# Kernel tuning notes

Measured on AMD Instinct MI355X. Metric: run time of the kernel, lower is better.

Reference implementation:

```python
import jax, jax.numpy as jnp
import numpy as np

N_NODES = 100000
D_IN = 128
D_OUT = 128
N_REL = 4
N_EDGES = 500000


def setup_inputs() -> dict:
    key = jax.random.key(0)
    k_x, k_e, k_w, k_b, k_ws, k_bs = jax.random.split(key, 6)
    x = jax.random.normal(k_x, (N_NODES, D_IN), dtype=jnp.float32)
    # edge_indices[r] = [2, E]: row 0 = source node ids, row 1 = target node ids
    edge_indices = jax.random.randint(k_e, (N_REL, 2, N_EDGES), 0, N_NODES, dtype=jnp.int32)
    scale = 1.0 / np.sqrt(D_IN)
    # per-relation Linear weights (out, in) and biases, like nn.Linear
    W = jax.random.uniform(k_w, (N_REL, D_OUT, D_IN), dtype=jnp.float32, minval=-scale, maxval=scale)
    b = jax.random.uniform(k_b, (N_REL, D_OUT), dtype=jnp.float32, minval=-scale, maxval=scale)
    W_sl = jax.random.uniform(k_ws, (D_OUT, D_IN), dtype=jnp.float32, minval=-scale, maxval=scale)
    b_sl = jax.random.uniform(k_bs, (D_OUT,), dtype=jnp.float32, minval=-scale, maxval=scale)
    return {"x": x, "edge_indices": edge_indices, "W": W, "b": b, "W_sl": W_sl, "b_sl": b_sl}


def reference(x, edge_indices, W, b, W_sl, b_sl):
    # gather source features per relation: [R, E, D_IN]
    src = edge_indices[:, 0]  # [R, E]
    tgt = edge_indices[:, 1]  # [R, E]
    xs = x[src]  # [R, E, D_IN]
    # per-relation linear (nn.Linear: x @ W.T + b): [R, E, D_OUT]
    msgs = jnp.einsum('red,rfd->ref', xs, W) + b[:, None, :]
    # scatter-add into per-relation node accumulators, then sum over relations
    agg = jax.vmap(lambda m, t: jax.ops.segment_sum(m, t, num_segments=N_NODES))(msgs, tgt)
    agg = agg.sum(axis=0)  # [N, D_OUT]
    # self loop
    agg = agg + x @ W_sl.T + b_sl
    return agg
```

## Files before the change

kernel.cpp:

```cpp
#include <hip/hip_runtime.h>
#include <hip/hip_bf16.h>

#define N_NODES 100000
#define D 128
#define N_REL 4
#define N_EDGES 500000
#define N_CNT (N_REL * N_NODES)
#define SCAN_CHUNK 1024
#define N_SCAN_BLK ((N_CNT + SCAN_CHUNK - 1) / SCAN_CHUNK)
#define SORT_MAX (N_REL * N_EDGES + 3 * N_CNT)
#define NXCD 8
#define NODES_PER_XCD (N_NODES / NXCD)

typedef __attribute__((ext_vector_type(8))) short bf16x8;
typedef __attribute__((ext_vector_type(4))) float f32x4;

__device__ __forceinline__ unsigned short f2bf(float f) {
    unsigned int u = __float_as_uint(f);
    u += 0x7fffu + ((u >> 16) & 1u);
    return (unsigned short)(u >> 16);
}

#define CVT_BLOCKS 6250
#define WB_BLOCKS 320
#define ZR_BLOCKS 1
#define HIST_BLOCKS (7813 * NXCD)
__global__ __launch_bounds__(256) void prep_kernel(const float* __restrict__ x,
                                                   const int* __restrict__ ei,
                                                   const float* __restrict__ W,
                                                   const float* __restrict__ W_sl,
                                                   ushort* __restrict__ xbf,
                                                   ushort* __restrict__ WbT,
                                                   int* __restrict__ cnt) {
    const int b = blockIdx.x, tid = threadIdx.x;
    if (b < CVT_BLOCKS) {
        size_t t = (size_t)b * 256 + tid;
        float4 v0 = ((const float4*)x)[t * 2];
        float4 v1 = ((const float4*)x)[t * 2 + 1];
        int4 o;
        o.x = ((int)f2bf(v0.y) << 16) | f2bf(v0.x);
        o.y = ((int)f2bf(v0.w) << 16) | f2bf(v0.z);
        o.z = ((int)f2bf(v1.y) << 16) | f2bf(v1.x);
        o.w = ((int)f2bf(v1.w) << 16) | f2bf(v1.z);
        ((int4*)xbf)[t] = o;
    } else if (b < CVT_BLOCKS + WB_BLOCKS) {
        int t = (b - CVT_BLOCKS) * 256 + tid;
        int f = t / 640;
        int k = t - f * 640;
        float v;
        if (k < 512) {
            int r = k >> 7, d = k & 127;
            v = W[((size_t)r * 128 + f) * 128 + d];
        } else {
            v = W_sl[(size_t)f * 128 + (k - 512)];
        }
        WbT[t] = f2bf(v);
    } else if (b < CVT_BLOCKS + WB_BLOCKS + ZR_BLOCKS) {
        if (tid < 16) ((uint4*)(xbf + (size_t)N_NODES * D))[tid] = make_uint4(0, 0, 0, 0);
    } else {
        int hb = b - CVT_BLOCKS - WB_BLOCKS - ZR_BLOCKS;
        int xcd = hb & 7;
        int t = (hb >> 3) * 256 + tid;
        if (t >= N_REL * N_EDGES) return;
        int r = t / N_EDGES;
        int e = t - r * N_EDGES;
        int tgt = ei[(size_t)r * 2 * N_EDGES + N_EDGES + e];
        if ((unsigned)(tgt - xcd * NODES_PER_XCD) < (unsigned)NODES_PER_XCD)
            atomicAdd(&cnt[r * N_NODES + tgt], 1);
    }
}

__global__ __launch_bounds__(256) void scanA(const int* __restrict__ cnt,
                                             int* __restrict__ foff,
                                             int* __restrict__ partials) {
    __shared__ int ps[256];
    int b = blockIdx.x, t = threadIdx.x;
    int i0 = b * SCAN_CHUNK + t * 4;
    int v[4];
#pragma unroll
    for (int q = 0; q < 4; ++q) v[q] = (i0 + q < N_CNT) ? ((cnt[i0 + q] + 3) & ~3) : 0;
    int s = v[0] + v[1] + v[2] + v[3];
    ps[t] = s;
    __syncthreads();
    for (int d = 1; d < 256; d <<= 1) {
        int u = (t >= d) ? ps[t - d] : 0;
        __syncthreads();
        ps[t] += u;
        __syncthreads();
    }
    if (t == 255) partials[b] = ps[255];
    int run = (t == 0) ? 0 : ps[t - 1];
#pragma unroll
    for (int q = 0; q < 4; ++q) {
        if (i0 + q < N_CNT) foff[i0 + q] = run;
        run += v[q];
    }
}

__global__ __launch_bounds__(256) void scanC(int* __restrict__ foff,
                                             const int* __restrict__ partials,
                                             const int* __restrict__ cnt,
                                             int* __restrict__ cur0,
                                             int* __restrict__ sorted) {
    __shared__ int red[256];
    const int b = blockIdx.x, t = threadIdx.x;
    const int pb = b >> 2;
    int s = 0;
    for (int j = t; j < pb; j += 256) s += partials[j];
    red[t] = s;
    __syncthreads();
    for (int d = 128; d > 0; d >>= 1) {
        if (t < d) red[t] += red[t + d];
        __syncthreads();
    }
    const int P = red[0];
    int i = b * 256 + t;
    if (i >= N_CNT) return;
    int base = foff[i] + P;
    foff[i] = base;
    cur0[i] = 0;
    int c = cnt[i];
    int cp = (c + 3) & ~3;
    for (int j = c; j < cp; ++j) sorted[base + j] = N_NODES;
    if (i == N_CNT - 1) foff[N_CNT] = base + cp;
}

__global__ __launch_bounds__(256) void bucket_kernel(const int* __restrict__ ei,
                                                     const int* __restrict__ foff,
                                                     int* __restrict__ cur0,
                                                     int* __restrict__ sorted) {
    const int xcd = blockIdx.x & 7;
    int t = (blockIdx.x >> 3) * 256 + threadIdx.x;
    if (t >= N_REL * N_EDGES) return;
    int r = t / N_EDGES;
    int e = t - r * N_EDGES;
    int tgt = ei[(size_t)r * 2 * N_EDGES + N_EDGES + e];
    if ((unsigned)(tgt - xcd * NODES_PER_XCD) >= (unsigned)NODES_PER_XCD) return;
    int src = ei[(size_t)r * 2 * N_EDGES + e];
    int i = r * N_NODES + tgt;
    int pos = foff[i] + atomicAdd(&cur0[i], 1);
    sorted[pos] = src;
}

__global__ __launch_bounds__(256) void gather_kernel(const ushort* __restrict__ xbf,
                                                     const int* __restrict__ sorted,
                                                     const int* __restrict__ foff,
                                                     unsigned int* __restrict__ buf) {
    int wid = (blockIdx.x * 256 + threadIdx.x) >> 6;
    wid = __builtin_amdgcn_readfirstlane(wid);
    const int lane = threadIdx.x & 63;
    const int p0 = wid * 4;
    int f0 = foff[p0], f1 = foff[p0 + 1], f2 = foff[p0 + 2], f3 = foff[p0 + 3], f4 = foff[p0 + 4];
#pragma unroll
    for (int pi = 0; pi < 4; ++pi) {
        int gb = (pi == 0) ? f0 : (pi == 1) ? f1 : (pi == 2) ? f2 : f3;
        int ge = (pi == 0) ? f1 : (pi == 1) ? f2 : (pi == 2) ? f3 : f4;
        float ax = 0.f, ay = 0.f;
        for (int g = gb; g < ge; g += 4) {
            int4 s = *(const int4*)(sorted + g);
            unsigned int u0 = ((const unsigned int*)(xbf + ((size_t)s.x << 7)))[lane];
            unsigned int u1 = ((const unsigned int*)(xbf + ((size_t)s.y << 7)))[lane];
            unsigned int u2 = ((const unsigned int*)(xbf + ((size_t)s.z << 7)))[lane];
            unsigned int u3 = ((const unsigned int*)(xbf + ((size_t)s.w << 7)))[lane];
            ax += __uint_as_float(u0 << 16) + __uint_as_float(u1 << 16)
                + __uint_as_float(u2 << 16) + __uint_as_float(u3 << 16);
            ay += __uint_as_float(u0 & 0xffff0000u) + __uint_as_float(u1 & 0xffff0000u)
                + __uint_as_float(u2 & 0xffff0000u) + __uint_as_float(u3 & 0xffff0000u);
        }
        buf[(size_t)(p0 + pi) * 64 + lane] = ((unsigned int)f2bf(ay) << 16) | f2bf(ax);
    }
}

__global__ __launch_bounds__(256) void gemm_kernel(const ushort* __restrict__ buf,
                                                   const ushort* __restrict__ xbf,
                                                   const ushort* __restrict__ WbT,
                                                   const int* __restrict__ cnt,
                                                   const float* __restrict__ bias,
                                                   const float* __restrict__ b_sl,
                                                   float* __restrict__ out) {
    __shared__ __align__(16) float SH[64 * 132];
    __shared__ float degS[4 * 128];
    __shared__ float biasS[4 * 128];
    __shared__ float bslS[128];
    ushort* As = (ushort*)SH;
    ushort* Bs = As + 128 * 64;

    const int tid = threadIdx.x;
    const int l = tid & 63, w = tid >> 6;
    const int wr = w >> 1, wc = w & 1;
    const int lr = l & 15, lq = l >> 4;
    const int n0 = blockIdx.x * 128;

#pragma unroll
    for (int it = 0; it < 2; ++it) {
        int idx = it * 256 + tid;
        int r = idx >> 7, row = idx & 127;
        int n = n0 + row;
        degS[idx] = (n < N_NODES) ? (float)cnt[r * N_NODES + n] : 0.f;
        biasS[idx] = bias[idx];
    }
    if (tid < 128) bslS[tid] = b_sl[tid];

    f32x4 acc[4][4];
#pragma unroll
    for (int mi = 0; mi < 4; ++mi)
#pragma unroll
        for (int ni = 0; ni < 4; ++ni) acc[mi][ni] = (f32x4){0.f, 0.f, 0.f, 0.f};

    for (int kt = 0; kt < 10; ++kt) {
        __syncthreads();
        const int region = kt >> 1;
        const int d0 = (kt & 1) * 64;
#pragma unroll
        for (int it = 0; it < 4; ++it) {
            int id = it * 256 + tid;
            int r_ = id >> 3, c16 = id & 7;
            int n = n0 + r_;
            if (n > N_NODES - 1) n = N_NODES - 1;
            const ushort* sp = (region < 4)
                ? (buf + (((size_t)region * N_NODES + n) << 7) + d0)
                : (xbf + ((size_t)n << 7) + d0);
            int4 va = *(const int4*)(sp + c16 * 8);
            *(int4*)(As + r_ * 64 + ((c16 ^ (r_ & 7)) << 3)) = va;
            int4 vb = *(const int4*)(WbT + (size_t)r_ * 640 + kt * 64 + c16 * 8);
            *(int4*)(Bs + r_ * 64 + ((c16 ^ (r_ & 7)) << 3)) = vb;
        }
        __syncthreads();
#pragma unroll
        for (int ks = 0; ks < 2; ++ks) {
            const int ch = ks * 4 + lq;
            const int chs = (ch ^ (lr & 7)) << 3;
            bf16x8 a[4], bb[4];
#pragma unroll
            for (int mi = 0; mi < 4; ++mi)
                a[mi] = *(const bf16x8*)(As + (wr * 64 + mi * 16 + lr) * 64 + chs);
#pragma unroll
            for (int ni = 0; ni < 4; ++ni)
                bb[ni] = *(const bf16x8*)(Bs + (wc * 64 + ni * 16 + lr) * 64 + chs);
#pragma unroll
            for (int mi = 0; mi < 4; ++mi)
#pragma unroll
                for (int ni = 0; ni < 4; ++ni)
                    acc[mi][ni] = __builtin_amdgcn_mfma_f32_16x16x32_bf16(a[mi], bb[ni], acc[mi][ni], 0, 0, 0);
        }
    }

    float bw[4][4], bsl_[4];
#pragma unroll
    for (int ni = 0; ni < 4; ++ni) {
        int f = wc * 64 + ni * 16 + lr;
        bsl_[ni] = bslS[f];
#pragma unroll
        for (int r = 0; r < 4; ++r) bw[ni][r] = biasS[r * 128 + f];
    }
    float* Cs = SH;
#pragma unroll
    for (int h = 0; h < 2; ++h) {
        __syncthreads();
        if (wr == h) {
#pragma unroll
            for (int mi = 0; mi < 4; ++mi)
#pragma unroll
                for (int q = 0; q < 4; ++q) {
                    int row = mi * 16 + lq * 4 + q;
                    int gr = h * 64 + row;
                    float d0_ = degS[gr], d1_ = degS[128 + gr], d2_ = degS[256 + gr], d3_ = degS[384 + gr];
#pragma unroll
                    for (int ni = 0; ni < 4; ++ni) {
                        int f = wc * 64 + ni * 16 + lr;
                        Cs[row * 132 + f] = acc[mi][ni][q] + d0_ * bw[ni][0] + d1_ * bw[ni][1]
                                          + d2_ * bw[ni][2] + d3_ * bw[ni][3] + bsl_[ni];
                    }
                }
        }
        __syncthreads();
#pragma unroll
        for (int it = 0; it < 8; ++it) {
            int idx = it * 256 + tid;
            int row = idx >> 5, c4 = idx & 31;
            int n = n0 + h * 64 + row;
            if (n < N_NODES)
                *(float4*)(out + (size_t)n * 128 + c4 * 4) = *(const float4*)(Cs + row * 132 + c4 * 4);
        }
    }
}

extern "C" void kernel_launch(void* const* d_in, const int* in_sizes, int n_in,
                              void* d_out, int out_size, void* d_ws, size_t ws_size,
                              hipStream_t stream) {
    const float* x    = (const float*)d_in[0];
    const int*   ei   = (const int*)d_in[1];
    const float* W    = (const float*)d_in[2];
    const float* b    = (const float*)d_in[3];
    const float* W_sl = (const float*)d_in[4];
    const float* b_sl = (const float*)d_in[5];
    float* out = (float*)d_out;

    int*          cnt      = (int*)d_ws;
    int*          cur0     = cnt + N_CNT;
    int*          foff     = cur0 + N_CNT;
    int*          partials = foff + N_CNT + 64;
    ushort*       WbT      = (ushort*)(partials + 512);
    ushort*       xbf      = WbT + 128 * 640;
    int*          sorted   = (int*)(xbf + (size_t)(N_NODES + 1) * D + 64);
    unsigned int* buf      = (unsigned int*)(sorted + SORT_MAX);

    hipMemsetAsync(cnt, 0, N_CNT * sizeof(int), stream);

    prep_kernel<<<CVT_BLOCKS + WB_BLOCKS + ZR_BLOCKS + HIST_BLOCKS, 256, 0, stream>>>(
        x, ei, W, W_sl, xbf, WbT, cnt);
    scanA<<<N_SCAN_BLK, 256, 0, stream>>>(cnt, foff, partials);
    scanC<<<(N_CNT + 255) / 256, 256, 0, stream>>>(foff, partials, cnt, cur0, sorted);
    bucket_kernel<<<((N_REL * N_EDGES + 255) / 256) * NXCD, 256, 0, stream>>>(ei, foff, cur0, sorted);
    gather_kernel<<<N_CNT / 16, 256, 0, stream>>>(xbf, sorted, foff, buf);
    gemm_kernel<<<(N_NODES + 127) / 128, 256, 0, stream>>>((const ushort*)buf, xbf, WbT, cnt, b, b_sl, out);
}
```

Measured before the change: 402.7 us.

## Simplify histogram to one pass and overlap first gather batch across segments

The histogram part of prep_kernel drops the per-XCD partitioning, launching one block per 256 edges instead of eight and doing global atomics without the XCD target filter. The gather kernel now issues the first int4 index load and first four row loads for all four segments up front, before the remaining per-segment loops, so more memory requests are in flight per wave. This trades XCD-local atomic locality for fewer redundant edge reads, and adds register pressure in the gather kernel.

```diff
diff --git a/kernel.cpp b/kernel.cpp
--- a/kernel.cpp
+++ b/kernel.cpp
@@ -24,7 +24,7 @@
 #define CVT_BLOCKS 6250
 #define WB_BLOCKS 320
 #define ZR_BLOCKS 1
-#define HIST_BLOCKS (7813 * NXCD)
+#define HIST_BLOCKS 7813
 __global__ __launch_bounds__(256) void prep_kernel(const float* __restrict__ x,
                                                    const int* __restrict__ ei,
                                                    const float* __restrict__ W,
@@ -58,15 +58,12 @@
     } else if (b < CVT_BLOCKS + WB_BLOCKS + ZR_BLOCKS) {
         if (tid < 16) ((uint4*)(xbf + (size_t)N_NODES * D))[tid] = make_uint4(0, 0, 0, 0);
     } else {
-        int hb = b - CVT_BLOCKS - WB_BLOCKS - ZR_BLOCKS;
-        int xcd = hb & 7;
-        int t = (hb >> 3) * 256 + tid;
+        int t = (b - CVT_BLOCKS - WB_BLOCKS - ZR_BLOCKS) * 256 + tid;
         if (t >= N_REL * N_EDGES) return;
         int r = t / N_EDGES;
         int e = t - r * N_EDGES;
         int tgt = ei[(size_t)r * 2 * N_EDGES + N_EDGES + e];
-        if ((unsigned)(tgt - xcd * NODES_PER_XCD) < (unsigned)NODES_PER_XCD)
-            atomicAdd(&cnt[r * N_NODES + tgt], 1);
+        atomicAdd(&cnt[r * N_NODES + tgt], 1);
     }
 }
 
@@ -142,6 +139,18 @@
     sorted[pos] = src;
 }
 
+__device__ __forceinline__ void gather4(const ushort* __restrict__ xbf, int4 s, int lane,
+                                        float& ax, float& ay) {
+    unsigned int u0 = ((const unsigned int*)(xbf + ((size_t)s.x << 7)))[lane];
+    unsigned int u1 = ((const unsigned int*)(xbf + ((size_t)s.y << 7)))[lane];
+    unsigned int u2 = ((const unsigned int*)(xbf + ((size_t)s.z << 7)))[lane];
+    unsigned int u3 = ((const unsigned int*)(xbf + ((size_t)s.w << 7)))[lane];
+    ax += __uint_as_float(u0 << 16) + __uint_as_float(u1 << 16)
+        + __uint_as_float(u2 << 16) + __uint_as_float(u3 << 16);
+    ay += __uint_as_float(u0 & 0xffff0000u) + __uint_as_float(u1 & 0xffff0000u)
+        + __uint_as_float(u2 & 0xffff0000u) + __uint_as_float(u3 & 0xffff0000u);
+}
+
 __global__ __launch_bounds__(256) void gather_kernel(const ushort* __restrict__ xbf,
                                                      const int* __restrict__ sorted,
                                                      const int* __restrict__ foff,
@@ -150,25 +159,28 @@
     wid = __builtin_amdgcn_readfirstlane(wid);
     const int lane = threadIdx.x & 63;
     const int p0 = wid * 4;
-    int f0 = foff[p0], f1 = foff[p0 + 1], f2 = foff[p0 + 2], f3 = foff[p0 + 3], f4 = foff[p0 + 4];
+    int f[5];
+#pragma unroll
+    for (int i = 0; i < 5; ++i) f[i] = foff[p0 + i];
+
+    float ax[4] = {0.f, 0.f, 0.f, 0.f}, ay[4] = {0.f, 0.f, 0.f, 0.f};
+    int4 s0[4];
+#pragma unroll
+    for (int pi = 0; pi < 4; ++pi)
+        if (f[pi + 1] > f[pi]) s0[pi] = *(const int4*)(sorted + f[pi]);
+#pragma unroll
+    for (int pi = 0; pi < 4; ++pi)
+        if (f[pi + 1] > f[pi]) gather4(xbf, s0[pi], lane, ax[pi], ay[pi]);
 #pragma unroll
     for (int pi = 0; pi < 4; ++pi) {
-        int gb = (pi == 0) ? f0 : (pi == 1) ? f1 : (pi == 2) ? f2 : f3;
-        int ge = (pi == 0) ? f1 : (pi == 1) ? f2 : (pi == 2) ? f3 : f4;
-        float ax = 0.f, ay = 0.f;
-        for (int g = gb; g < ge; g += 4) {
+        for (int g = f[pi] + 4; g < f[pi + 1]; g += 4) {
             int4 s = *(const int4*)(sorted + g);
-            unsigned int u0 = ((const unsigned int*)(xbf + ((size_t)s.x << 7)))[lane];
-            unsigned int u1 = ((const unsigned int*)(xbf + ((size_t)s.y << 7)))[lane];
-            unsigned int u2 = ((const unsigned int*)(xbf + ((size_t)s.z << 7)))[lane];
-            unsigned int u3 = ((const unsigned int*)(xbf + ((size_t)s.w << 7)))[lane];
-            ax += __uint_as_float(u0 << 16) + __uint_as_float(u1 << 16)
-                + __uint_as_float(u2 << 16) + __uint_as_float(u3 << 16);
-            ay += __uint_as_float(u0 & 0xffff0000u) + __uint_as_float(u1 & 0xffff0000u)
-                + __uint_as_float(u2 & 0xffff0000u) + __uint_as_float(u3 & 0xffff0000u);
-        }
-        buf[(size_t)(p0 + pi) * 64 + lane] = ((unsigned int)f2bf(ay) << 16) | f2bf(ax);
-    }
+            gather4(xbf, s, lane, ax[pi], ay[pi]);
+        }
+    }
+#pragma unroll
+    for (int pi = 0; pi < 4; ++pi)
+        buf[(size_t)(p0 + pi) * 64 + lane] = ((unsigned int)f2bf(ay[pi]) << 16) | f2bf(ax[pi]);
 }
 
 __global__ __launch_bounds__(256) void gemm_kernel(const ushort* __restrict__ buf,
```

Result: no change. 404.2 us (+0.4%).
